# Kernel tuning notes

Measured on AMD Instinct MI355X. Metric: run time of the kernel, lower is better.

The kernel has to match this reference:

```python
import jax, jax.numpy as jnp
import numpy as np

FP8_DTYPE = jnp.float8_e4m3fn
FP8_MAX = float(jnp.finfo(FP8_DTYPE).max)  # 448.0


def fp8_quantize(x):
    # per-tensor dynamic scaling: scale = fp8_max / amax(|x|)
    amax = jnp.maximum(jnp.max(jnp.abs(x)), 1e-12)
    scale = FP8_MAX / amax
    q = jnp.clip(x * scale, -FP8_MAX, FP8_MAX).astype(FP8_DTYPE)
    return q, (1.0 / scale).astype(jnp.float32)  # return reciprocal (dequant) scale


def setup_inputs() -> dict:
    key = jax.random.key(0)
    k1, k2, k3 = jax.random.split(key, 3)
    M, K, N = 4096, 4096, 11008
    inp = jax.random.normal(k1, (M, K), dtype=jnp.float32)
    weight = jax.random.normal(k2, (N, K), dtype=jnp.float32) * 0.02
    bias = jax.random.normal(k3, (N,), dtype=jnp.float32) * 0.01
    return {"input": inp, "weight": weight, "bias": bias}


def reference(input, weight, bias):
    # weight quantization (done once at init in the torch module)
    qweight, w_scale = fp8_quantize(weight)
    # dynamic per-tensor input quantization each forward
    qinput, in_scale = fp8_quantize(input)
    # scaled_mm: out = scale_a * scale_b * (qa @ qb) + bias, in out_dtype (fp32)
    acc = jnp.einsum(
        "mk,nk->mn",
        qinput.astype(jnp.float32),
        qweight.astype(jnp.float32),
    )
    out = acc * (in_scale * w_scale) + bias[None, :]
    return out
```

## Files before the change

### kernel.cpp

```cpp
#include <hip/hip_runtime.h>
#include <stdint.h>

typedef float f32x4 __attribute__((ext_vector_type(4)));
typedef int   i32x4 __attribute__((ext_vector_type(4)));
typedef int   i32x8 __attribute__((ext_vector_type(8)));

#define AS1 __attribute__((address_space(1)))
#define AS3 __attribute__((address_space(3)))

__device__ __forceinline__ void async_copy16(const void* g, void* l) {
    __builtin_amdgcn_global_load_lds((AS1 void*)(g), (AS3 void*)(l), 16, 0, 0);
}

__global__ void init_kernel(unsigned* amaxs) {
    if (threadIdx.x < 2) amaxs[threadIdx.x] = 0u;
}

__global__ __launch_bounds__(256) void amax2_kernel(
    const float4* __restrict__ x0, int n40,
    const float4* __restrict__ x1, int n41,
    int nb0, unsigned* __restrict__ amaxs)
{
    __shared__ float red[4];
    const float4* x; int n4; unsigned* dst; int bid, nb;
    if ((int)blockIdx.x < nb0) {
        x = x0; n4 = n40; dst = amaxs + 0; bid = blockIdx.x; nb = nb0;
    } else {
        x = x1; n4 = n41; dst = amaxs + 1; bid = blockIdx.x - nb0; nb = gridDim.x - nb0;
    }
    float m = 0.0f;
    int idx = bid * 256 + threadIdx.x;
    int stride = nb * 256;
    for (int i = idx; i < n4; i += stride) {
        float4 v = x[i];
        m = fmaxf(fmaxf(m, fmaxf(fabsf(v.x), fabsf(v.y))),
                  fmaxf(fabsf(v.z), fabsf(v.w)));
    }
#pragma unroll
    for (int off = 32; off > 0; off >>= 1)
        m = fmaxf(m, __shfl_down(m, off));
    if ((threadIdx.x & 63) == 0) red[threadIdx.x >> 6] = m;
    __syncthreads();
    if (threadIdx.x == 0) {
        m = fmaxf(fmaxf(red[0], red[1]), fmaxf(red[2], red[3]));
        atomicMax(dst, __float_as_uint(m));
    }
}

__global__ __launch_bounds__(256) void quant2_kernel(
    const float4* __restrict__ x0, int n40,
    const float4* __restrict__ x1, int n41,
    int nb0, const unsigned* __restrict__ amaxs,
    unsigned* __restrict__ q0, unsigned* __restrict__ q1)
{
    const float4* x; int n4; unsigned* q; int bid, nb; float amax;
    if ((int)blockIdx.x < nb0) {
        x = x0; n4 = n40; q = q0; bid = blockIdx.x; nb = nb0;
        amax = __uint_as_float(amaxs[0]);
    } else {
        x = x1; n4 = n41; q = q1; bid = blockIdx.x - nb0; nb = gridDim.x - nb0;
        amax = __uint_as_float(amaxs[1]);
    }
    const float s = 448.0f / fmaxf(amax, 1e-12f);
    int idx = bid * 256 + threadIdx.x;
    int stride = nb * 256;
    for (int i = idx; i < n4; i += stride) {
        float4 v = x[i];
        float a = fminf(fmaxf(v.x * s, -448.0f), 448.0f);
        float b = fminf(fmaxf(v.y * s, -448.0f), 448.0f);
        float c = fminf(fmaxf(v.z * s, -448.0f), 448.0f);
        float d = fminf(fmaxf(v.w * s, -448.0f), 448.0f);
        int p = 0;
        p = __builtin_amdgcn_cvt_pk_fp8_f32(a, b, p, false);
        p = __builtin_amdgcn_cvt_pk_fp8_f32(c, d, p, true);
        q[i] = (unsigned)p;
    }
}

#define RING 9
#define STEPB 8192

__global__ __launch_bounds__(512, 2) void gemm_fp8(
    const uint8_t* __restrict__ qA,
    const uint8_t* __restrict__ qB,
    const float*   __restrict__ bias,
    const unsigned* __restrict__ amaxs,
    float* __restrict__ out,
    int M, int N, int K)
{
    __shared__ uint8_t lds[2 * RING * STEPB];

    const int tid  = threadIdx.x;
    const int lane = tid & 63;
    const int wave = tid >> 6;
    const int wm   = wave >> 2;
    const int wn   = wave & 3;

    const int ntiles = N >> 8;
    const int per    = (int)gridDim.x >> 3;
    const int swz    = ((int)blockIdx.x & 7) * per + ((int)blockIdx.x >> 3);
    const int mtile  = swz / ntiles;
    const int ntile  = swz - mtile * ntiles;

    const int li   = lane & 15;
    const int lj   = lane >> 4;
    const int jx16 = lj << 4;
    const int ai32 = li << 5;

    uint8_t* ldsA = lds;
    uint8_t* ldsB = lds + RING * STEPB;
    const int wl = wave << 10;

    const uint8_t* gApan = qA + (size_t)(mtile << 8) * K;
    const uint8_t* gBpan = qB + (size_t)(ntile << 8) * K;

    int off[4];
#pragma unroll
    for (int g = 0; g < 4; ++g) {
        int x = tid ^ g;
        off[g] = (x >> 1) * K + (x & 1) * 16;
    }

#define STAGE(u_, su_, g_) do {                                              \
        async_copy16(gApan + (off[(g_)] + ((u_) << 5)),                      \
                     ldsA + ((su_) * STEPB + wl));                           \
        async_copy16(gBpan + (off[(g_)] + ((u_) << 5)),                      \
                     ldsB + ((su_) * STEPB + wl));                           \
    } while (0)

#define LDFRAG(dst_, base_, rowc_) do {                                      \
        int _o = (((rowc_) + ai32) ^ jx16);                                  \
        i32x4 _lo = *(const i32x4*)((base_) + _o);                           \
        i32x4 _hi = *(const i32x4*)((base_) + (_o ^ 16));                    \
        (dst_) = __builtin_shufflevector(_lo, _hi, 0, 1, 2, 3, 4, 5, 6, 7);  \
    } while (0)

#define MFMA(acc_, a_, b_)                                                   \
    (acc_) = __builtin_amdgcn_mfma_scale_f32_16x16x128_f8f6f4(               \
        (a_), (b_), (acc_), 0, 0, 0, 0x7F7F7F7F, 0, 0x7F7F7F7F)

    STAGE(0, 0, 0); STAGE(1, 1, 1); STAGE(2, 2, 2); STAGE(3, 3, 3); STAGE(4, 4, 0);
    asm volatile("s_waitcnt vmcnt(2)" ::: "memory");
    __builtin_amdgcn_s_barrier();
    asm volatile("" ::: "memory");

    f32x4 acc[8][4] = {};
    i32x8 afr[4], bfr[4];

    const int rAc = wm << 12;
    const int rBc = wn << 11;
    const int NSTEP = K >> 7;
    const int NSU   = K >> 5;

    int s4 = 0;
#pragma unroll 1
    for (int t = 0; t < NSTEP; ++t) {
        int sl = s4 + lj; if (sl >= RING) sl -= RING;
        const uint8_t* rdA = ldsA + sl * STEPB;
        const uint8_t* rdB = ldsB + sl * STEPB;
        const int u0 = (t << 2) + 5;

        LDFRAG(afr[0], rdA, rAc + 0 * 512);
        LDFRAG(afr[1], rdA, rAc + 1 * 512);
        LDFRAG(afr[2], rdA, rAc + 2 * 512);
        LDFRAG(afr[3], rdA, rAc + 3 * 512);
        LDFRAG(bfr[0], rdB, rBc + 0 * 512);
        LDFRAG(bfr[1], rdB, rBc + 1 * 512);
        if (u0 < NSU) { int su = s4 + 5; if (su >= RING) su -= RING; STAGE(u0, su, 1); }
        __builtin_amdgcn_s_barrier();
        __builtin_amdgcn_s_setprio(1);
#pragma unroll
        for (int fi = 0; fi < 4; ++fi) {
            MFMA(acc[fi][0], afr[fi], bfr[0]);
            MFMA(acc[fi][1], afr[fi], bfr[1]);
        }
        __builtin_amdgcn_s_setprio(0);
        __builtin_amdgcn_s_barrier();

        LDFRAG(bfr[2], rdB, rBc + 2 * 512);
        LDFRAG(bfr[3], rdB, rBc + 3 * 512);
        if (u0 + 1 < NSU) { int su = s4 + 6; if (su >= RING) su -= RING; STAGE(u0 + 1, su, 2); }
        __builtin_amdgcn_s_barrier();
        __builtin_amdgcn_s_setprio(1);
#pragma unroll
        for (int fi = 0; fi < 4; ++fi) {
            MFMA(acc[fi][2], afr[fi], bfr[2]);
            MFMA(acc[fi][3], afr[fi], bfr[3]);
        }
        __builtin_amdgcn_s_setprio(0);
        __builtin_amdgcn_s_barrier();

        LDFRAG(afr[0], rdA, rAc + 2048 + 0 * 512);
        LDFRAG(afr[1], rdA, rAc + 2048 + 1 * 512);
        LDFRAG(afr[2], rdA, rAc + 2048 + 2 * 512);
        LDFRAG(afr[3], rdA, rAc + 2048 + 3 * 512);
        if (u0 + 2 < NSU) { int su = s4 + 7; if (su >= RING) su -= RING; STAGE(u0 + 2, su, 3); }
        __builtin_amdgcn_s_barrier();
        __builtin_amdgcn_s_setprio(1);
#pragma unroll
        for (int fi = 0; fi < 4; ++fi) {
            MFMA(acc[4 + fi][2], afr[fi], bfr[2]);
            MFMA(acc[4 + fi][3], afr[fi], bfr[3]);
        }
        __builtin_amdgcn_s_setprio(0);
        __builtin_amdgcn_s_barrier();

        if (u0 + 3 < NSU) { int su = s4 + 8; if (su >= RING) su -= RING; STAGE(u0 + 3, su, 0); }
        __builtin_amdgcn_s_barrier();
        __builtin_amdgcn_s_setprio(1);
#pragma unroll
        for (int fi = 0; fi < 4; ++fi) {
            MFMA(acc[4 + fi][0], afr[fi], bfr[0]);
            MFMA(acc[4 + fi][1], afr[fi], bfr[1]);
        }
        __builtin_amdgcn_s_setprio(0);

        if (t == NSTEP - 2)      asm volatile("s_waitcnt vmcnt(0)" ::: "memory");
        else if (t <  NSTEP - 2) asm volatile("s_waitcnt vmcnt(2)" ::: "memory");
        __builtin_amdgcn_s_barrier();
        asm volatile("" ::: "memory");

        s4 += 4; if (s4 >= RING) s4 -= RING;
    }

    const float amax_a = fmaxf(__uint_as_float(amaxs[0]), 1e-12f);
    const float amax_w = fmaxf(__uint_as_float(amaxs[1]), 1e-12f);
    const float scale = (amax_a * amax_w) * (1.0f / (448.0f * 448.0f));

    const int row0 = (mtile << 8) + (wm << 7) + (lj << 2);
    const int col0 = (ntile << 8) + (wn << 6) + li;
#pragma unroll
    for (int fj = 0; fj < 4; ++fj) {
        const int col = col0 + fj * 16;
        const float bv = bias[col];
#pragma unroll
        for (int fi = 0; fi < 8; ++fi) {
            const int row = row0 + fi * 16;
#pragma unroll
            for (int r = 0; r < 4; ++r)
                out[(size_t)(row + r) * N + col] = acc[fi][fj][r] * scale + bv;
        }
    }
#undef STAGE
#undef LDFRAG
#undef MFMA
}

extern "C" void kernel_launch(void* const* d_in, const int* in_sizes, int n_in,
                              void* d_out, int out_size, void* d_ws, size_t ws_size,
                              hipStream_t stream) {
    const float* inp  = (const float*)d_in[0];
    const float* wgt  = (const float*)d_in[1];
    const float* bias = (const float*)d_in[2];
    float* out = (float*)d_out;

    const int N = in_sizes[2];
    const int K = in_sizes[1] / N;
    const int M = in_sizes[0] / K;

    unsigned* amaxs = (unsigned*)d_ws;
    uint8_t* qin = (uint8_t*)d_ws + 256;
    uint8_t* qw  = qin + (size_t)M * K;

    const int n4i = M * K / 4;
    const int n4w = N * K / 4;
    const int nb_i = 768, nb_w = 2048;

    init_kernel<<<1, 64, 0, stream>>>(amaxs);
    amax2_kernel<<<nb_i + nb_w, 256, 0, stream>>>(
        (const float4*)inp, n4i, (const float4*)wgt, n4w, nb_i, amaxs);
    quant2_kernel<<<nb_i + nb_w, 256, 0, stream>>>(
        (const float4*)inp, n4i, (const float4*)wgt, n4w, nb_i, amaxs,
        (unsigned*)qin, (unsigned*)qw);

    const int grid = (M >> 8) * (N >> 8);
    gemm_fp8<<<grid, 512, 0, stream>>>(qin, qw, bias, amaxs, out, M, N, K);
}
```

Before: 629.4 us.

## Fuse amax and quantize into a cooperative kernel and relax GEMM barriers

Replaces the init, amax and quantize launches with a single cooperative kernel that uses grid syncs between zeroing, amax reduction and quantization, and unrolls the loads by four. In the GEMM main loop, all four STAGE async copies are issued up front and most per-substep s_barriers are removed, so global-to-LDS copies overlap with MFMA work and there are fewer syncs. This saves launch overhead and barrier stalls. The price is fewer prep blocks (1024), possible L2 reuse loss, and a risk of LDS races, since ring slots are refilled with less synchronization.

```diff
diff --git a/kernel.cpp b/kernel.cpp
--- a/kernel.cpp
+++ b/kernel.cpp
@@ -1,5 +1,8 @@
 #include <hip/hip_runtime.h>
+#include <hip/hip_cooperative_groups.h>
 #include <stdint.h>
+
+namespace cg = cooperative_groups;
 
 typedef float f32x4 __attribute__((ext_vector_type(4)));
 typedef int   i32x4 __attribute__((ext_vector_type(4)));
@@ -12,26 +15,54 @@
     __builtin_amdgcn_global_load_lds((AS1 void*)(g), (AS3 void*)(l), 16, 0, 0);
 }
 
-__global__ void init_kernel(unsigned* amaxs) {
-    if (threadIdx.x < 2) amaxs[threadIdx.x] = 0u;
-}
-
-__global__ __launch_bounds__(256) void amax2_kernel(
-    const float4* __restrict__ x0, int n40,
-    const float4* __restrict__ x1, int n41,
-    int nb0, unsigned* __restrict__ amaxs)
+__device__ __forceinline__ unsigned pack_fp8x4(float4 v, float s) {
+    float a = fminf(fmaxf(v.x * s, -448.0f), 448.0f);
+    float b = fminf(fmaxf(v.y * s, -448.0f), 448.0f);
+    float c = fminf(fmaxf(v.z * s, -448.0f), 448.0f);
+    float d = fminf(fmaxf(v.w * s, -448.0f), 448.0f);
+    int p = 0;
+    p = __builtin_amdgcn_cvt_pk_fp8_f32(a, b, p, false);
+    p = __builtin_amdgcn_cvt_pk_fp8_f32(c, d, p, true);
+    return (unsigned)p;
+}
+
+__global__ __launch_bounds__(256, 4) void prep_kernel(
+    const float4* __restrict__ inp, int n4i,
+    const float4* __restrict__ wgt, int n4w,
+    int nb_i, unsigned* __restrict__ amaxs,
+    unsigned* __restrict__ qi, unsigned* __restrict__ qw)
 {
     __shared__ float red[4];
-    const float4* x; int n4; unsigned* dst; int bid, nb;
-    if ((int)blockIdx.x < nb0) {
-        x = x0; n4 = n40; dst = amaxs + 0; bid = blockIdx.x; nb = nb0;
-    } else {
-        x = x1; n4 = n41; dst = amaxs + 1; bid = blockIdx.x - nb0; nb = gridDim.x - nb0;
-    }
+    const int tid = threadIdx.x;
+    const int bid = blockIdx.x;
+    const bool isw = bid >= nb_i;
+    const float4* x = isw ? wgt : inp;
+    const int n4   = isw ? n4w : n4i;
+    unsigned* q    = isw ? qw  : qi;
+    const int lb   = isw ? bid - nb_i : bid;
+    const int lnb  = isw ? (int)gridDim.x - nb_i : nb_i;
+
+    cg::grid_group grid = cg::this_grid();
+
+    if (bid == 0 && tid < 2) amaxs[tid] = 0u;
+    grid.sync();
+
+    const int idx = lb * 256 + tid;
+    const int stride = lnb * 256;
     float m = 0.0f;
-    int idx = bid * 256 + threadIdx.x;
-    int stride = nb * 256;
-    for (int i = idx; i < n4; i += stride) {
+    int i = idx;
+    for (; i + 3 * stride < n4; i += 4 * stride) {
+        float4 v0 = x[i];
+        float4 v1 = x[i + stride];
+        float4 v2 = x[i + 2 * stride];
+        float4 v3 = x[i + 3 * stride];
+        float m0 = fmaxf(fmaxf(fabsf(v0.x), fabsf(v0.y)), fmaxf(fabsf(v0.z), fabsf(v0.w)));
+        float m1 = fmaxf(fmaxf(fabsf(v1.x), fabsf(v1.y)), fmaxf(fabsf(v1.z), fabsf(v1.w)));
+        float m2 = fmaxf(fmaxf(fabsf(v2.x), fabsf(v2.y)), fmaxf(fabsf(v2.z), fabsf(v2.w)));
+        float m3 = fmaxf(fmaxf(fabsf(v3.x), fabsf(v3.y)), fmaxf(fabsf(v3.z), fabsf(v3.w)));
+        m = fmaxf(m, fmaxf(fmaxf(m0, m1), fmaxf(m2, m3)));
+    }
+    for (; i < n4; i += stride) {
         float4 v = x[i];
         m = fmaxf(fmaxf(m, fmaxf(fabsf(v.x), fabsf(v.y))),
                   fmaxf(fabsf(v.z), fabsf(v.w)));
@@ -39,42 +70,28 @@
 #pragma unroll
     for (int off = 32; off > 0; off >>= 1)
         m = fmaxf(m, __shfl_down(m, off));
-    if ((threadIdx.x & 63) == 0) red[threadIdx.x >> 6] = m;
+    if ((tid & 63) == 0) red[tid >> 6] = m;
     __syncthreads();
-    if (threadIdx.x == 0) {
+    if (tid == 0) {
         m = fmaxf(fmaxf(red[0], red[1]), fmaxf(red[2], red[3]));
-        atomicMax(dst, __float_as_uint(m));
-    }
-}
-
-__global__ __launch_bounds__(256) void quant2_kernel(
-    const float4* __restrict__ x0, int n40,
-    const float4* __restrict__ x1, int n41,
-    int nb0, const unsigned* __restrict__ amaxs,
-    unsigned* __restrict__ q0, unsigned* __restrict__ q1)
-{
-    const float4* x; int n4; unsigned* q; int bid, nb; float amax;
-    if ((int)blockIdx.x < nb0) {
-        x = x0; n4 = n40; q = q0; bid = blockIdx.x; nb = nb0;
-        amax = __uint_as_float(amaxs[0]);
-    } else {
-        x = x1; n4 = n41; q = q1; bid = blockIdx.x - nb0; nb = gridDim.x - nb0;
-        amax = __uint_as_float(amaxs[1]);
-    }
-    const float s = 448.0f / fmaxf(amax, 1e-12f);
-    int idx = bid * 256 + threadIdx.x;
-    int stride = nb * 256;
-    for (int i = idx; i < n4; i += stride) {
-        float4 v = x[i];
-        float a = fminf(fmaxf(v.x * s, -448.0f), 448.0f);
-        float b = fminf(fmaxf(v.y * s, -448.0f), 448.0f);
-        float c = fminf(fmaxf(v.z * s, -448.0f), 448.0f);
-        float d = fminf(fmaxf(v.w * s, -448.0f), 448.0f);
-        int p = 0;
-        p = __builtin_amdgcn_cvt_pk_fp8_f32(a, b, p, false);
-        p = __builtin_amdgcn_cvt_pk_fp8_f32(c, d, p, true);
-        q[i] = (unsigned)p;
-    }
+        atomicMax(amaxs + (isw ? 1 : 0), __float_as_uint(m));
+    }
+    grid.sync();
+
+    const float amax = fmaxf(__uint_as_float(amaxs[isw ? 1 : 0]), 1e-12f);
+    const float s = 448.0f / amax;
+    i = idx;
+    for (; i + 3 * stride < n4; i += 4 * stride) {
+        float4 v0 = x[i];
+        float4 v1 = x[i + stride];
+        float4 v2 = x[i + 2 * stride];
+        float4 v3 = x[i + 3 * stride];
+        q[i]              = pack_fp8x4(v0, s);
+        q[i + stride]     = pack_fp8x4(v1, s);
+        q[i + 2 * stride] = pack_fp8x4(v2, s);
+        q[i + 3 * stride] = pack_fp8x4(v3, s);
+    }
+    for (; i < n4; i += stride) q[i] = pack_fp8x4(x[i], s);
 }
 
 #define RING 9
@@ -160,14 +177,17 @@
         const uint8_t* rdB = ldsB + sl * STEPB;
         const int u0 = (t << 2) + 5;
 
+        { int su = s4 + 5; if (su >= RING) su -= RING; if (u0     < NSU) STAGE(u0,     su, 1); }
+        { int su = s4 + 6; if (su >= RING) su -= RING; if (u0 + 1 < NSU) STAGE(u0 + 1, su, 2); }
+        { int su = s4 + 7; if (su >= RING) su -= RING; if (u0 + 2 < NSU) STAGE(u0 + 2, su, 3); }
+        { int su = s4 + 8; if (su >= RING) su -= RING; if (u0 + 3 < NSU) STAGE(u0 + 3, su, 0); }
+
         LDFRAG(afr[0], rdA, rAc + 0 * 512);
         LDFRAG(afr[1], rdA, rAc + 1 * 512);
         LDFRAG(afr[2], rdA, rAc + 2 * 512);
         LDFRAG(afr[3], rdA, rAc + 3 * 512);
         LDFRAG(bfr[0], rdB, rBc + 0 * 512);
         LDFRAG(bfr[1], rdB, rBc + 1 * 512);
-        if (u0 < NSU) { int su = s4 + 5; if (su >= RING) su -= RING; STAGE(u0, su, 1); }
-        __builtin_amdgcn_s_barrier();
         __builtin_amdgcn_s_setprio(1);
 #pragma unroll
         for (int fi = 0; fi < 4; ++fi) {
@@ -175,12 +195,9 @@
             MFMA(acc[fi][1], afr[fi], bfr[1]);
         }
         __builtin_amdgcn_s_setprio(0);
-        __builtin_amdgcn_s_barrier();
 
         LDFRAG(bfr[2], rdB, rBc + 2 * 512);
         LDFRAG(bfr[3], rdB, rBc + 3 * 512);
-        if (u0 + 1 < NSU) { int su = s4 + 6; if (su >= RING) su -= RING; STAGE(u0 + 1, su, 2); }
-        __builtin_amdgcn_s_barrier();
         __builtin_amdgcn_s_setprio(1);
 #pragma unroll
         for (int fi = 0; fi < 4; ++fi) {
@@ -188,26 +205,17 @@
             MFMA(acc[fi][3], afr[fi], bfr[3]);
         }
         __builtin_amdgcn_s_setprio(0);
-        __builtin_amdgcn_s_barrier();
 
         LDFRAG(afr[0], rdA, rAc + 2048 + 0 * 512);
         LDFRAG(afr[1], rdA, rAc + 2048 + 1 * 512);
         LDFRAG(afr[2], rdA, rAc + 2048 + 2 * 512);
         LDFRAG(afr[3], rdA, rAc + 2048 + 3 * 512);
-        if (u0 + 2 < NSU) { int su = s4 + 7; if (su >= RING) su -= RING; STAGE(u0 + 2, su, 3); }
-        __builtin_amdgcn_s_barrier();
         __builtin_amdgcn_s_setprio(1);
 #pragma unroll
         for (int fi = 0; fi < 4; ++fi) {
             MFMA(acc[4 + fi][2], afr[fi], bfr[2]);
             MFMA(acc[4 + fi][3], afr[fi], bfr[3]);
         }
-        __builtin_amdgcn_s_setprio(0);
-        __builtin_amdgcn_s_barrier();
-
-        if (u0 + 3 < NSU) { int su = s4 + 8; if (su >= RING) su -= RING; STAGE(u0 + 3, su, 0); }
-        __builtin_amdgcn_s_barrier();
-        __builtin_amdgcn_s_setprio(1);
 #pragma unroll
         for (int fi = 0; fi < 4; ++fi) {
             MFMA(acc[4 + fi][0], afr[fi], bfr[0]);
@@ -262,17 +270,19 @@
     uint8_t* qin = (uint8_t*)d_ws + 256;
     uint8_t* qw  = qin + (size_t)M * K;
 
-    const int n4i = M * K / 4;
-    const int n4w = N * K / 4;
-    const int nb_i = 768, nb_w = 2048;
-
-    init_kernel<<<1, 64, 0, stream>>>(amaxs);
-    amax2_kernel<<<nb_i + nb_w, 256, 0, stream>>>(
-        (const float4*)inp, n4i, (const float4*)wgt, n4w, nb_i, amaxs);
-    quant2_kernel<<<nb_i + nb_w, 256, 0, stream>>>(
-        (const float4*)inp, n4i, (const float4*)wgt, n4w, nb_i, amaxs,
-        (unsigned*)qin, (unsigned*)qw);
-
-    const int grid = (M >> 8) * (N >> 8);
+    int n4i = M * K / 4;
+    int n4w = N * K / 4;
+    int nb_i = 256;
+
+    const float4* inp4 = (const float4*)inp;
+    const float4* wgt4 = (const float4*)wgt;
+    unsigned* qi_p = (unsigned*)qin;
+    unsigned* qw_p = (unsigned*)qw;
+    void* args[] = { (void*)&inp4, (void*)&n4i, (void*)&wgt4, (void*)&n4w,
+                     (void*)&nb_i, (void*)&amaxs, (void*)&qi_p, (void*)&qw_p };
+    hipLaunchCooperativeKernel((const void*)prep_kernel, dim3(1024), dim3(256),
+                               args, 0, stream);
+
+    dim3 grid((M >> 8) * (N >> 8));
     gemm_fp8<<<grid, 512, 0, stream>>>(qin, qw, bias, amaxs, out, M, N, K);
 }
```

Result: slower. 778.5 us (+23.7%).
